# Kernel tuning notes

Measured on AMD Instinct MI355X. Metric: run time of the kernel, lower is better.

## Reference

```python
import jax, jax.numpy as jnp
import numpy as np

N_ATOMS = 100000
N_MOLS = 5000
IN_F = 1008
H1, H2, H3 = 256, 192, 160
OUT_C = 1
ELEMS = np.array([1, 6, 7, 8, 9])  # H, C, N, O, F
ALPHA = 0.1


def setup_inputs() -> dict:
    key = jax.random.key(0)
    ks = jax.random.split(key, 12)
    zidx = jax.random.randint(ks[0], (N_ATOMS,), 0, 5)
    z = jnp.asarray(ELEMS)[zidx].astype(jnp.int64)
    features = jax.random.normal(ks[1], (N_ATOMS, IN_F), dtype=jnp.float32)
    batch = jnp.sort(jax.random.randint(ks[2], (N_ATOMS,), 0, N_MOLS)).astype(jnp.int64)
    # Stacked per-element MLP params: leading axis = 5 element types (H,C,N,O,F)
    def w(k, shape, fan_in):
        return jax.random.normal(k, shape, dtype=jnp.float32) / np.sqrt(fan_in)
    W1 = w(ks[3], (5, IN_F, H1), IN_F); b1 = jnp.zeros((5, H1), jnp.float32)
    W2 = w(ks[4], (5, H1, H2), H1);     b2 = jnp.zeros((5, H2), jnp.float32)
    W3 = w(ks[5], (5, H2, H3), H2);     b3 = jnp.zeros((5, H3), jnp.float32)
    W4 = w(ks[6], (5, H3, OUT_C), H3);  b4 = jnp.zeros((5, OUT_C), jnp.float32)
    return {"z": z, "features": features, "batch": batch, "n_mols": N_MOLS,
            "W1": W1, "b1": b1, "W2": W2, "b2": b2,
            "W3": W3, "b3": b3, "W4": W4, "b4": b4}


def _celu(x):
    return jax.nn.celu(x, alpha=ALPHA)


def reference(z, features, batch, n_mols, W1, b1, W2, b2, W3, b3, W4, b4):
    # Per-element-type MLPs run over all atoms (t = 5 element types), then the
    # atom's true type is selected via a one-hot mask -- equivalent to the
    # gather -> per-type MLP -> scatter-back in the torch forward.
    h = _celu(jnp.einsum('nf,tfh->tnh', features, W1) + b1[:, None, :])
    h = _celu(jnp.einsum('tnh,thg->tng', h, W2) + b2[:, None, :])
    h = _celu(jnp.einsum('tng,tgk->tnk', h, W3) + b3[:, None, :])
    v_all = jnp.einsum('tnk,tko->tno', h, W4) + b4[:, None, :]  # [5, N, out]
    onehot = (z[None, :] == jnp.asarray(ELEMS)[:, None]).astype(features.dtype)  # [5, N]
    v = jnp.einsum('tn,tno->no', onehot, v_all)  # [N, out]
    u = jax.ops.segment_sum(v, batch, num_segments=n_mols)  # [n_mols, out]
    return u
```

## Files before the change

kernel.cpp:

```cpp
#include <hip/hip_runtime.h>
#include <stdint.h>

#define NF    1008
#define NH1   256
#define NH2   192
#define NH3   160
#define MT    64
#define CELU_ALPHA 0.1f

typedef __attribute__((ext_vector_type(8))) __bf16 bf16x8;
typedef __attribute__((ext_vector_type(4))) float  f32x4;

#define W1F_OFF   0u
#define W2F_OFF   2621440u
#define W3F_OFF   3112960u
#define META_OFF  3420160u
#define SORT_OFF  3420288u

__device__ __forceinline__ unsigned short f2bf(float f) {
  union { float f; uint32_t u; } v; v.f = f;
  uint32_t u = v.u;
  uint32_t r = u + 0x7FFFu + ((u >> 16) & 1u);
  return (unsigned short)(r >> 16);
}

__device__ __forceinline__ float celu_f(float x) {
  return x > 0.f ? x : CELU_ALPHA * (__expf(x * (1.f / CELU_ALPHA)) - 1.f);
}

__device__ __forceinline__ int ztype(int z) {
  return z == 1 ? 0 : z == 6 ? 1 : z == 7 ? 2 : z == 8 ? 3 : 4;
}

__global__ void prep_and_hist(const float* __restrict__ W1, const float* __restrict__ W2,
                              const float* __restrict__ W3,
                              unsigned short* __restrict__ w1f, unsigned short* __restrict__ w2f,
                              unsigned short* __restrict__ w3f,
                              const int* __restrict__ z, int n, int* __restrict__ counts) {
  int bid = blockIdx.x;
  int tid = threadIdx.x;
  if (bid >= 425) {
    __shared__ int h[5];
    if (tid < 5) h[tid] = 0;
    __syncthreads();
    int i = (bid - 425) * 256 + tid;
    if (i < n) atomicAdd(&h[ztype(z[i])], 1);
    __syncthreads();
    if (tid < 5 && h[tid]) atomicAdd(&counts[tid], h[tid]);
    return;
  }
  const float* src; unsigned short* dst; int K, N, NJ, NKS, kt, nt;
  if (bid < 320) {
    int t = bid / 64, r = bid % 64; kt = r / 4; nt = r % 4;
    src = W1 + (size_t)t * NF * NH1; dst = w1f + (size_t)t * 16 * 32 * 512;
    K = NF; N = NH1; NJ = 16; NKS = 32;
  } else if (bid < 380) {
    int b = bid - 320; int t = b / 12, r = b % 12; kt = r / 3; nt = r % 3;
    src = W2 + (size_t)t * NH1 * NH2; dst = w2f + (size_t)t * 12 * 8 * 512;
    K = NH1; N = NH2; NJ = 12; NKS = 8;
  } else {
    int b = bid - 380; int t = b / 9, r = b % 9; kt = r / 3; nt = r % 3;
    src = W3 + (size_t)t * NH2 * NH3; dst = w3f + (size_t)t * 10 * 6 * 512;
    K = NH2; N = NH3; NJ = 10; NKS = 6;
  }
  __shared__ float tile[64][65];
  int k0 = kt * 64, n0 = nt * 64;
  {
    int nl = tid & 63, kb = tid >> 6;
    #pragma unroll
    for (int i = 0; i < 16; ++i) {
      int kl = kb + 4 * i;
      int k = k0 + kl, nn = n0 + nl;
      tile[kl][nl] = (k < K && nn < N) ? src[(size_t)k * N + nn] : 0.f;
    }
  }
  __syncthreads();
  {
    #pragma unroll
    for (int i = 0; i < 16; ++i) {
      int o = tid + 256 * i;
      int e  = o & 7;
      int l  = (o >> 3) & 63;
      int ks2 = (o >> 9) & 1;
      int j2  = o >> 10;
      int kl = ks2 * 32 + ((l >> 4) << 3) + e;
      int nl = j2 * 16 + (l & 15);
      int gj  = (n0 >> 4) + j2;
      int gks = (k0 >> 5) + ks2;
      if (gj < NJ && gks < NKS)
        dst[((size_t)gj * NKS + gks) * 512 + (o & 511)] = f2bf(tile[kl][nl]);
    }
  }
}

__global__ void plan_tiles(const int* __restrict__ counts, int* __restrict__ atom_base,
                           int* __restrict__ tile_base) {
  if (threadIdx.x == 0 && blockIdx.x == 0) {
    int a = 0, tb = 0;
    for (int t = 0; t < 5; ++t) {
      atom_base[t] = a; tile_base[t] = tb;
      a += counts[t]; tb += (counts[t] + MT - 1) / MT;
    }
    atom_base[5] = a; tile_base[5] = tb;
  }
}

__global__ void scatter_atoms(const int* __restrict__ z, int n,
                              const int* __restrict__ atom_base, int* __restrict__ cursors,
                              int* __restrict__ sorted) {
  int i = blockIdx.x * blockDim.x + threadIdx.x;
  int lane = threadIdx.x & 63;
  int t = (i < n) ? ztype(z[i]) : -1;
  #pragma unroll
  for (int tt = 0; tt < 5; ++tt) {
    unsigned long long mask = __ballot(t == tt);
    if (t == tt) {
      int leader = __ffsll((long long)mask) - 1;
      int rank = __popcll(mask & ((1ull << lane) - 1ull));
      int base = 0;
      if (lane == leader) base = atomicAdd(&cursors[tt], (int)__popcll(mask));
      base = __shfl(base, leader);
      sorted[atom_base[tt] + base + rank] = i;
    }
  }
}

__global__ __launch_bounds__(512, 4) void fcnn_main(
    const float* __restrict__ feat, const int* __restrict__ batch,
    const unsigned short* __restrict__ w1f, const unsigned short* __restrict__ w2f,
    const unsigned short* __restrict__ w3f, const float* __restrict__ W4,
    const float* __restrict__ b1, const float* __restrict__ b2,
    const float* __restrict__ b3, const float* __restrict__ b4,
    const int* __restrict__ atom_base, const int* __restrict__ tile_base,
    const int* __restrict__ sorted_idx, float* __restrict__ out) {
  __shared__ __align__(16) unsigned char smem[65792];
  unsigned short* A0  = (unsigned short*)smem;
  unsigned short* A1  = (unsigned short*)(smem + 32768);
  unsigned short* h1s = (unsigned short*)smem;
  unsigned short* h2s = (unsigned short*)(smem + 32768);
  unsigned short* h3s = (unsigned short*)smem;
  int* lgid = (int*)(smem + 65536);

  const int bid = blockIdx.x;
  if (bid >= tile_base[5]) return;
  int t = 0;
  #pragma unroll
  for (int i = 0; i < 4; ++i) if (bid >= tile_base[i + 1]) t = i + 1;
  const int m0 = atom_base[t] + (bid - tile_base[t]) * MT;
  const int rows = min(MT, atom_base[t + 1] - m0);

  const int tid = threadIdx.x;
  const int lane = tid & 63;
  const int w = tid >> 6;
  const int col = lane & 15;
  const int q = lane >> 4;
  const int lx8 = lane << 3;
  const int swzR = (col & 7) << 3;

  if (tid < MT) lgid[tid] = (tid < rows) ? sorted_idx[m0 + tid] : -1;
  __syncthreads();

  const int srow = tid >> 3;
  const int sl = tid & 7;
  const int sg = lgid[srow];
  const float* fsrc = (sg >= 0) ? (feat + (size_t)sg * NF) : feat;
  const int swzW = (srow & 7) << 3;

  const unsigned short* w1p0 = w1f + (size_t)t * 16 * 32 * 512 + (size_t)w * 32 * 512 + lx8;
  const unsigned short* w1p1 = w1p0 + 8 * 32 * 512;

  f32x4 acc[4][2];
  #pragma unroll
  for (int a = 0; a < 4; ++a)
    #pragma unroll
    for (int b = 0; b < 2; ++b) acc[a][b] = (f32x4){0.f, 0.f, 0.f, 0.f};

  f32x4 nv[8];
  #pragma unroll
  for (int i = 0; i < 8; ++i) {
    int k = (sl + 8 * i) * 4;
    nv[i] = (sg >= 0 && k < NF) ? *(const f32x4*)(fsrc + k) : (f32x4){0.f, 0.f, 0.f, 0.f};
  }
  #pragma unroll
  for (int i = 0; i < 8; ++i) {
    int c = sl + 8 * i;
    ushort4 pk;
    pk.x = f2bf(nv[i][0]); pk.y = f2bf(nv[i][1]); pk.z = f2bf(nv[i][2]); pk.w = f2bf(nv[i][3]);
    *(ushort4*)(A0 + srow * 256 + (((c << 2)) ^ swzW)) = pk;
  }
  __syncthreads();

  #pragma unroll 1
  for (int kc = 0; kc < 4; ++kc) {
    if (kc < 3) {
      #pragma unroll
      for (int i = 0; i < 8; ++i) {
        int k = (kc + 1) * 256 + (sl + 8 * i) * 4;
        nv[i] = (sg >= 0 && k < NF) ? *(const f32x4*)(fsrc + k) : (f32x4){0.f, 0.f, 0.f, 0.f};
      }
    }
    const unsigned short* ab = (kc & 1) ? A1 : A0;
    #pragma unroll
    for (int ks = 0; ks < 8; ++ks) {
      bf16x8 af[4];
      #pragma unroll
      for (int im = 0; im < 4; ++im)
        af[im] = *(const bf16x8*)(ab + (im * 16 + col) * 256 + ((ks * 32 + q * 8) ^ swzR));
      bf16x8 bf0 = *(const bf16x8*)(w1p0 + (size_t)(kc * 8 + ks) * 512);
      bf16x8 bf1 = *(const bf16x8*)(w1p1 + (size_t)(kc * 8 + ks) * 512);
      #pragma unroll
      for (int im = 0; im < 4; ++im) {
        acc[im][0] = __builtin_amdgcn_mfma_f32_16x16x32_bf16(af[im], bf0, acc[im][0], 0, 0, 0);
        acc[im][1] = __builtin_amdgcn_mfma_f32_16x16x32_bf16(af[im], bf1, acc[im][1], 0, 0, 0);
      }
    }
    if (kc < 3) {
      unsigned short* dst = (kc & 1) ? A0 : A1;
      #pragma unroll
      for (int i = 0; i < 8; ++i) {
        int c = sl + 8 * i;
        ushort4 pk;
        pk.x = f2bf(nv[i][0]); pk.y = f2bf(nv[i][1]); pk.z = f2bf(nv[i][2]); pk.w = f2bf(nv[i][3]);
        *(ushort4*)(dst + srow * 256 + (((c << 2)) ^ swzW)) = pk;
      }
    }
    __syncthreads();
  }

  #pragma unroll
  for (int jj = 0; jj < 2; ++jj) {
    int n = (w + 8 * jj) * 16 + col;
    float bias = b1[t * NH1 + n];
    #pragma unroll
    for (int im = 0; im < 4; ++im)
      #pragma unroll
      for (int r = 0; r < 4; ++r) {
        int row = im * 16 + q * 4 + r;
        h1s[row * 256 + (n ^ ((row & 7) << 3))] = f2bf(celu_f(acc[im][jj][r] + bias));
      }
  }
  __syncthreads();

  f32x4 acc2[4][2];
  #pragma unroll
  for (int a = 0; a < 4; ++a)
    #pragma unroll
    for (int b = 0; b < 2; ++b) acc2[a][b] = (f32x4){0.f, 0.f, 0.f, 0.f};
  const unsigned short* w2p0 = w2f + (size_t)t * 12 * 8 * 512 + (size_t)w * 8 * 512 + lx8;
  const unsigned short* w2p1 = w2p0 + 8 * 8 * 512;
  #pragma unroll
  for (int ks = 0; ks < 8; ++ks) {
    bf16x8 af[4];
    #pragma unroll
    for (int im = 0; im < 4; ++im)
      af[im] = *(const bf16x8*)(h1s + (im * 16 + col) * 256 + ((ks * 32 + q * 8) ^ swzR));
    bf16x8 bf0 = *(const bf16x8*)(w2p0 + (size_t)ks * 512);
    #pragma unroll
    for (int im = 0; im < 4; ++im)
      acc2[im][0] = __builtin_amdgcn_mfma_f32_16x16x32_bf16(af[im], bf0, acc2[im][0], 0, 0, 0);
    if (w < 4) {
      bf16x8 bf1 = *(const bf16x8*)(w2p1 + (size_t)ks * 512);
      #pragma unroll
      for (int im = 0; im < 4; ++im)
        acc2[im][1] = __builtin_amdgcn_mfma_f32_16x16x32_bf16(af[im], bf1, acc2[im][1], 0, 0, 0);
    }
  }
  #pragma unroll
  for (int jj = 0; jj < 2; ++jj) {
    int j = w + 8 * jj;
    if (j < 12) {
      int n = j * 16 + col;
      float bias = b2[t * NH2 + n];
      #pragma unroll
      for (int im = 0; im < 4; ++im)
        #pragma unroll
        for (int r = 0; r < 4; ++r) {
          int row = im * 16 + q * 4 + r;
          h2s[row * 192 + (n ^ ((row & 7) << 3))] = f2bf(celu_f(acc2[im][jj][r] + bias));
        }
    }
  }
  __syncthreads();

  f32x4 acc3[4][2];
  #pragma unroll
  for (int a = 0; a < 4; ++a)
    #pragma unroll
    for (int b = 0; b < 2; ++b) acc3[a][b] = (f32x4){0.f, 0.f, 0.f, 0.f};
  const unsigned short* w3p0 = w3f + (size_t)t * 10 * 6 * 512 + (size_t)w * 6 * 512 + lx8;
  const unsigned short* w3p1 = w3p0 + 8 * 6 * 512;
  #pragma unroll
  for (int ks = 0; ks < 6; ++ks) {
    bf16x8 af[4];
    #pragma unroll
    for (int im = 0; im < 4; ++im)
      af[im] = *(const bf16x8*)(h2s + (im * 16 + col) * 192 + ((ks * 32 + q * 8) ^ swzR));
    bf16x8 bf0 = *(const bf16x8*)(w3p0 + (size_t)ks * 512);
    #pragma unroll
    for (int im = 0; im < 4; ++im)
      acc3[im][0] = __builtin_amdgcn_mfma_f32_16x16x32_bf16(af[im], bf0, acc3[im][0], 0, 0, 0);
    if (w < 2) {
      bf16x8 bf1 = *(const bf16x8*)(w3p1 + (size_t)ks * 512);
      #pragma unroll
      for (int im = 0; im < 4; ++im)
        acc3[im][1] = __builtin_amdgcn_mfma_f32_16x16x32_bf16(af[im], bf1, acc3[im][1], 0, 0, 0);
    }
  }
  #pragma unroll
  for (int jj = 0; jj < 2; ++jj) {
    int j = w + 8 * jj;
    if (j < 10) {
      int n = j * 16 + col;
      float bias = b3[t * NH3 + n];
      #pragma unroll
      for (int im = 0; im < 4; ++im)
        #pragma unroll
        for (int r = 0; r < 4; ++r) {
          int row = im * 16 + q * 4 + r;
          h3s[row * 192 + (n ^ ((row & 7) << 3))] = f2bf(celu_f(acc3[im][jj][r] + bias));
        }
    }
  }
  __syncthreads();

  {
    int a = tid >> 3, p = tid & 7;
    float v = 0.f;
    if (a < rows) {
      const float* wp = W4 + t * NH3;
      int aswz = (a & 7) << 3;
      #pragma unroll
      for (int c0 = 0; c0 < 3; ++c0) {
        int c = p + 8 * c0;
        if (c < 20) {
          bf16x8 hv = *(const bf16x8*)(h3s + a * 192 + ((c * 8) ^ aswz));
          #pragma unroll
          for (int j = 0; j < 8; ++j) v += (float)hv[j] * wp[c * 8 + j];
        }
      }
    }
    v += __shfl_xor(v, 1);
    v += __shfl_xor(v, 2);
    v += __shfl_xor(v, 4);
    if (p == 0 && a < rows) {
      int g = lgid[a];
      atomicAdd(&out[batch[g]], v + b4[t]);
    }
  }
}

extern "C" void kernel_launch(void* const* d_in, const int* in_sizes, int n_in,
                              void* d_out, int out_size, void* d_ws, size_t ws_size,
                              hipStream_t stream) {
  const int*   z    = (const int*)d_in[0];
  const float* feat = (const float*)d_in[1];
  const int*   bat  = (const int*)d_in[2];
  const float* W1 = (const float*)d_in[4];
  const float* b1 = (const float*)d_in[5];
  const float* W2 = (const float*)d_in[6];
  const float* b2 = (const float*)d_in[7];
  const float* W3 = (const float*)d_in[8];
  const float* b3 = (const float*)d_in[9];
  const float* W4 = (const float*)d_in[10];
  const float* b4 = (const float*)d_in[11];
  const int n = in_sizes[0];

  unsigned char* ws = (unsigned char*)d_ws;
  unsigned short* w1f = (unsigned short*)(ws + W1F_OFF);
  unsigned short* w2f = (unsigned short*)(ws + W2F_OFF);
  unsigned short* w3f = (unsigned short*)(ws + W3F_OFF);
  int* meta = (int*)(ws + META_OFF);
  int* counts    = meta;
  int* atom_base = meta + 8;
  int* tile_base = meta + 16;
  int* cursors   = meta + 24;
  int* sorted    = (int*)(ws + SORT_OFF);

  hipMemsetAsync(meta, 0, 128, stream);
  hipMemsetAsync(d_out, 0, (size_t)out_size * sizeof(float), stream);

  int nb = (n + 255) / 256;
  prep_and_hist<<<425 + nb, 256, 0, stream>>>(W1, W2, W3, w1f, w2f, w3f, z, n, counts);
  plan_tiles<<<1, 64, 0, stream>>>(counts, atom_base, tile_base);
  scatter_atoms<<<nb, 256, 0, stream>>>(z, n, atom_base, cursors, sorted);
  int max_tiles = n / MT + 6;
  fcnn_main<<<max_tiles, 512, 0, stream>>>(feat, bat, w1f, w2f, w3f, W4,
                                           b1, b2, b3, b4,
                                           atom_base, tile_base, sorted,
                                           (float*)d_out);
  (void)n_in; (void)ws_size;
}
```

Measured before the change: 740.2 us.

## Drop plan_tiles kernel, halve K-chunk size and prefetch W1 fragments into registers

Removes the single-thread plan_tiles launch; each block and the scatter kernel now compute the type offsets inline from counts. The layer-1 K loop is reworked into 8 chunks of 128 instead of 4 of 256, which shrinks the staging buffers and shared memory from about 64 KB to 56 KB. W1 fragments for the next chunk are now prefetched into registers alongside the feature loads. MFMA sections are wrapped in s_setprio, and the software f2bf rounding is replaced by native __bf16 conversion. The change trades more barriers per tile and extra register pressure for less launch overhead, possibly better occupancy, and better overlap of global loads with MFMA work.

```diff
diff --git a/kernel.cpp b/kernel.cpp
--- a/kernel.cpp
+++ b/kernel.cpp
@@ -9,6 +9,7 @@
 #define CELU_ALPHA 0.1f
 
 typedef __attribute__((ext_vector_type(8))) __bf16 bf16x8;
+typedef __attribute__((ext_vector_type(4))) __bf16 bf16x4;
 typedef __attribute__((ext_vector_type(4))) float  f32x4;
 
 #define W1F_OFF   0u
@@ -93,24 +94,13 @@
   }
 }
 
-__global__ void plan_tiles(const int* __restrict__ counts, int* __restrict__ atom_base,
-                           int* __restrict__ tile_base) {
-  if (threadIdx.x == 0 && blockIdx.x == 0) {
-    int a = 0, tb = 0;
-    for (int t = 0; t < 5; ++t) {
-      atom_base[t] = a; tile_base[t] = tb;
-      a += counts[t]; tb += (counts[t] + MT - 1) / MT;
-    }
-    atom_base[5] = a; tile_base[5] = tb;
-  }
-}
-
 __global__ void scatter_atoms(const int* __restrict__ z, int n,
-                              const int* __restrict__ atom_base, int* __restrict__ cursors,
+                              const int* __restrict__ counts, int* __restrict__ cursors,
                               int* __restrict__ sorted) {
   int i = blockIdx.x * blockDim.x + threadIdx.x;
   int lane = threadIdx.x & 63;
   int t = (i < n) ? ztype(z[i]) : -1;
+  int ab = 0;
   #pragma unroll
   for (int tt = 0; tt < 5; ++tt) {
     unsigned long long mask = __ballot(t == tt);
@@ -120,8 +110,9 @@
       int base = 0;
       if (lane == leader) base = atomicAdd(&cursors[tt], (int)__popcll(mask));
       base = __shfl(base, leader);
-      sorted[atom_base[tt] + base + rank] = i;
-    }
+      sorted[ab + base + rank] = i;
+    }
+    ab += counts[tt];
   }
 }
 
@@ -131,23 +122,28 @@
     const unsigned short* __restrict__ w3f, const float* __restrict__ W4,
     const float* __restrict__ b1, const float* __restrict__ b2,
     const float* __restrict__ b3, const float* __restrict__ b4,
-    const int* __restrict__ atom_base, const int* __restrict__ tile_base,
-    const int* __restrict__ sorted_idx, float* __restrict__ out) {
-  __shared__ __align__(16) unsigned char smem[65792];
-  unsigned short* A0  = (unsigned short*)smem;
-  unsigned short* A1  = (unsigned short*)(smem + 32768);
-  unsigned short* h1s = (unsigned short*)smem;
-  unsigned short* h2s = (unsigned short*)(smem + 32768);
-  unsigned short* h3s = (unsigned short*)smem;
-  int* lgid = (int*)(smem + 65536);
+    const int* __restrict__ counts, const int* __restrict__ sorted_idx,
+    float* __restrict__ out) {
+  __shared__ __align__(16) unsigned char smem[57600];
+  __bf16* A0v = (__bf16*)smem;
+  __bf16* A1v = (__bf16*)(smem + 16384);
+  __bf16* h1s = (__bf16*)smem;
+  __bf16* h2s = (__bf16*)(smem + 32768);
+  __bf16* h3s = (__bf16*)smem;
+  int* lgid = (int*)(smem + 57344);
 
   const int bid = blockIdx.x;
-  if (bid >= tile_base[5]) return;
-  int t = 0;
-  #pragma unroll
-  for (int i = 0; i < 4; ++i) if (bid >= tile_base[i + 1]) t = i + 1;
-  const int m0 = atom_base[t] + (bid - tile_base[t]) * MT;
-  const int rows = min(MT, atom_base[t + 1] - m0);
+  int t = 0, abase = 0, tbase = 0, cend = 0, total_t = 0, total_a = 0;
+  #pragma unroll
+  for (int i = 0; i < 5; ++i) {
+    int ci = counts[i];
+    int nti = (ci + MT - 1) / MT;
+    if (bid >= total_t && bid < total_t + nti) { t = i; abase = total_a; tbase = total_t; cend = total_a + ci; }
+    total_t += nti; total_a += ci;
+  }
+  if (bid >= total_t) return;
+  const int m0 = abase + (bid - tbase) * MT;
+  const int rows = min(MT, cend - m0);
 
   const int tid = threadIdx.x;
   const int lane = tid & 63;
@@ -157,12 +153,10 @@
   const int lx8 = lane << 3;
   const int swzR = (col & 7) << 3;
 
-  if (tid < MT) lgid[tid] = (tid < rows) ? sorted_idx[m0 + tid] : -1;
-  __syncthreads();
-
   const int srow = tid >> 3;
   const int sl = tid & 7;
-  const int sg = lgid[srow];
+  const int sg = (srow < rows) ? sorted_idx[m0 + srow] : -1;
+  if (tid < MT) lgid[tid] = (tid < rows) ? sorted_idx[m0 + tid] : -1;
   const float* fsrc = (sg >= 0) ? (feat + (size_t)sg * NF) : feat;
   const int swzW = (srow & 7) << 3;
 
@@ -175,54 +169,58 @@
     #pragma unroll
     for (int b = 0; b < 2; ++b) acc[a][b] = (f32x4){0.f, 0.f, 0.f, 0.f};
 
-  f32x4 nv[8];
-  #pragma unroll
-  for (int i = 0; i < 8; ++i) {
-    int k = (sl + 8 * i) * 4;
-    nv[i] = (sg >= 0 && k < NF) ? *(const f32x4*)(fsrc + k) : (f32x4){0.f, 0.f, 0.f, 0.f};
-  }
-  #pragma unroll
-  for (int i = 0; i < 8; ++i) {
-    int c = sl + 8 * i;
-    ushort4 pk;
-    pk.x = f2bf(nv[i][0]); pk.y = f2bf(nv[i][1]); pk.z = f2bf(nv[i][2]); pk.w = f2bf(nv[i][3]);
-    *(ushort4*)(A0 + srow * 256 + (((c << 2)) ^ swzW)) = pk;
-  }
+  f32x4 nv[4];
+  bf16x8 wf[8];
+
+  auto feat_issue = [&](int kc1) {
+    #pragma unroll
+    for (int i = 0; i < 4; ++i) {
+      int k = kc1 * 128 + ((sl + 8 * i) << 2);
+      nv[i] = (sg >= 0 && k < NF) ? *(const f32x4*)(fsrc + k) : (f32x4){0.f, 0.f, 0.f, 0.f};
+    }
+  };
+  auto pack_to = [&](__bf16* dstp) {
+    #pragma unroll
+    for (int i = 0; i < 4; ++i) {
+      int c4 = (sl + 8 * i) << 2;
+      bf16x4 pk = { (__bf16)nv[i][0], (__bf16)nv[i][1], (__bf16)nv[i][2], (__bf16)nv[i][3] };
+      *(bf16x4*)(dstp + srow * 128 + (c4 ^ swzW)) = pk;
+    }
+  };
+  auto wf_issue = [&](int kc1) {
+    #pragma unroll
+    for (int ks = 0; ks < 4; ++ks) {
+      wf[ks]     = *(const bf16x8*)(w1p0 + (size_t)(kc1 * 4 + ks) * 512);
+      wf[4 + ks] = *(const bf16x8*)(w1p1 + (size_t)(kc1 * 4 + ks) * 512);
+    }
+  };
+
+  feat_issue(0);
+  pack_to(A0v);
+  wf_issue(0);
   __syncthreads();
 
   #pragma unroll 1
-  for (int kc = 0; kc < 4; ++kc) {
-    if (kc < 3) {
-      #pragma unroll
-      for (int i = 0; i < 8; ++i) {
-        int k = (kc + 1) * 256 + (sl + 8 * i) * 4;
-        nv[i] = (sg >= 0 && k < NF) ? *(const f32x4*)(fsrc + k) : (f32x4){0.f, 0.f, 0.f, 0.f};
+  for (int kc = 0; kc < 8; ++kc) {
+    const __bf16* ab = (kc & 1) ? A1v : A0v;
+    if (kc < 7) feat_issue(kc + 1);
+    __builtin_amdgcn_s_setprio(1);
+    #pragma unroll
+    for (int ks = 0; ks < 4; ++ks) {
+      bf16x8 af[4];
+      #pragma unroll
+      for (int im = 0; im < 4; ++im)
+        af[im] = *(const bf16x8*)(ab + (im * 16 + col) * 128 + ((ks * 32 + q * 8) ^ swzR));
+      #pragma unroll
+      for (int im = 0; im < 4; ++im) {
+        acc[im][0] = __builtin_amdgcn_mfma_f32_16x16x32_bf16(af[im], wf[ks],     acc[im][0], 0, 0, 0);
+        acc[im][1] = __builtin_amdgcn_mfma_f32_16x16x32_bf16(af[im], wf[4 + ks], acc[im][1], 0, 0, 0);
       }
     }
-    const unsigned short* ab = (kc & 1) ? A1 : A0;
-    #pragma unroll
-    for (int ks = 0; ks < 8; ++ks) {
-      bf16x8 af[4];
-      #pragma unroll
-      for (int im = 0; im < 4; ++im)
-        af[im] = *(const bf16x8*)(ab + (im * 16 + col) * 256 + ((ks * 32 + q * 8) ^ swzR));
-      bf16x8 bf0 = *(const bf16x8*)(w1p0 + (size_t)(kc * 8 + ks) * 512);
-      bf16x8 bf1 = *(const bf16x8*)(w1p1 + (size_t)(kc * 8 + ks) * 512);
-      #pragma unroll
-      for (int im = 0; im < 4; ++im) {
-        acc[im][0] = __builtin_amdgcn_mfma_f32_16x16x32_bf16(af[im], bf0, acc[im][0], 0, 0, 0);
-        acc[im][1] = __builtin_amdgcn_mfma_f32_16x16x32_bf16(af[im], bf1, acc[im][1], 0, 0, 0);
-      }
-    }
-    if (kc < 3) {
-      unsigned short* dst = (kc & 1) ? A0 : A1;
-      #pragma unroll
-      for (int i = 0; i < 8; ++i) {
-        int c = sl + 8 * i;
-        ushort4 pk;
-        pk.x = f2bf(nv[i][0]); pk.y = f2bf(nv[i][1]); pk.z = f2bf(nv[i][2]); pk.w = f2bf(nv[i][3]);
-        *(ushort4*)(dst + srow * 256 + (((c << 2)) ^ swzW)) = pk;
-      }
+    __builtin_amdgcn_s_setprio(0);
+    if (kc < 7) {
+      pack_to((kc & 1) ? A0v : A1v);
+      wf_issue(kc + 1);
     }
     __syncthreads();
   }
@@ -236,7 +234,7 @@
       #pragma unroll
       for (int r = 0; r < 4; ++r) {
         int row = im * 16 + q * 4 + r;
-        h1s[row * 256 + (n ^ ((row & 7) << 3))] = f2bf(celu_f(acc[im][jj][r] + bias));
+        h1s[row * 256 + (n ^ ((row & 7) << 3))] = (__bf16)celu_f(acc[im][jj][r] + bias);
       }
   }
   __syncthreads();
@@ -248,6 +246,7 @@
     for (int b = 0; b < 2; ++b) acc2[a][b] = (f32x4){0.f, 0.f, 0.f, 0.f};
   const unsigned short* w2p0 = w2f + (size_t)t * 12 * 8 * 512 + (size_t)w * 8 * 512 + lx8;
   const unsigned short* w2p1 = w2p0 + 8 * 8 * 512;
+  __builtin_amdgcn_s_setprio(1);
   #pragma unroll
   for (int ks = 0; ks < 8; ++ks) {
     bf16x8 af[4];
@@ -265,6 +264,7 @@
         acc2[im][1] = __builtin_amdgcn_mfma_f32_16x16x32_bf16(af[im], bf1, acc2[im][1], 0, 0, 0);
     }
   }
+  __builtin_amdgcn_s_setprio(0);
   #pragma unroll
   for (int jj = 0; jj < 2; ++jj) {
     int j = w + 8 * jj;
@@ -276,7 +276,7 @@
         #pragma unroll
         for (int r = 0; r < 4; ++r) {
           int row = im * 16 + q * 4 + r;
-          h2s[row * 192 + (n ^ ((row & 7) << 3))] = f2bf(celu_f(acc2[im][jj][r] + bias));
+          h2s[row * 192 + (n ^ ((row & 7) << 3))] = (__bf16)celu_f(acc2[im][jj][r] + bias);
         }
     }
   }
@@ -289,6 +289,7 @@
     for (int b = 0; b < 2; ++b) acc3[a][b] = (f32x4){0.f, 0.f, 0.f, 0.f};
   const unsigned short* w3p0 = w3f + (size_t)t * 10 * 6 * 512 + (size_t)w * 6 * 512 + lx8;
   const unsigned short* w3p1 = w3p0 + 8 * 6 * 512;
+  __builtin_amdgcn_s_setprio(1);
   #pragma unroll
   for (int ks = 0; ks < 6; ++ks) {
     bf16x8 af[4];
@@ -306,6 +307,7 @@
         acc3[im][1] = __builtin_amdgcn_mfma_f32_16x16x32_bf16(af[im], bf1, acc3[im][1], 0, 0, 0);
     }
   }
+  __builtin_amdgcn_s_setprio(0);
   #pragma unroll
   for (int jj = 0; jj < 2; ++jj) {
     int j = w + 8 * jj;
@@ -317,7 +319,7 @@
         #pragma unroll
         for (int r = 0; r < 4; ++r) {
           int row = im * 16 + q * 4 + r;
-          h3s[row * 192 + (n ^ ((row & 7) << 3))] = f2bf(celu_f(acc3[im][jj][r] + bias));
+          h3s[row * 192 + (n ^ ((row & 7) << 3))] = (__bf16)celu_f(acc3[im][jj][r] + bias);
         }
     }
   }
@@ -371,8 +373,6 @@
   unsigned short* w3f = (unsigned short*)(ws + W3F_OFF);
   int* meta = (int*)(ws + META_OFF);
   int* counts    = meta;
-  int* atom_base = meta + 8;
-  int* tile_base = meta + 16;
   int* cursors   = meta + 24;
   int* sorted    = (int*)(ws + SORT_OFF);
 
@@ -381,12 +381,11 @@
 
   int nb = (n + 255) / 256;
   prep_and_hist<<<425 + nb, 256, 0, stream>>>(W1, W2, W3, w1f, w2f, w3f, z, n, counts);
-  plan_tiles<<<1, 64, 0, stream>>>(counts, atom_base, tile_base);
-  scatter_atoms<<<nb, 256, 0, stream>>>(z, n, atom_base, cursors, sorted);
+  scatter_atoms<<<nb, 256, 0, stream>>>(z, n, counts, cursors, sorted);
   int max_tiles = n / MT + 6;
   fcnn_main<<<max_tiles, 512, 0, stream>>>(feat, bat, w1f, w2f, w3f, W4,
                                            b1, b2, b3, b4,
-                                           atom_base, tile_base, sorted,
+                                           counts, sorted,
                                            (float*)d_out);
   (void)n_in; (void)ws_size;
 }
```

New measurement: 711.0 us. -3.9%, faster.
